# Performance work log

Measured on AMD Instinct MI355X. Metric: run time of the kernel, lower is better.

Reference implementation:

```python
import jax, jax.numpy as jnp
import numpy as np

# Standard 2D morphsnakes structuring elements (4 line filters), matching the
# repo-level global `filters` used by LSNet2.
_SE = np.zeros((4, 3, 3), dtype=np.float32)
_SE[0, 1, :] = 1.0           # horizontal line
_SE[1, :, 1] = 1.0           # vertical line
_SE[2] = np.eye(3, dtype=np.float32)          # main diagonal
_SE[3] = np.eye(3, dtype=np.float32)[::-1]    # anti-diagonal


def _dilate_stack(x, filts):
    # per-pixel: max over 3x3 window of (zero-padded x + filt), for every filter
    H, W = x.shape
    p = jnp.pad(x, 1)
    m = jnp.full((filts.shape[0], H, W), -jnp.inf, x.dtype)
    for k in range(3):
        for l in range(3):
            m = jnp.maximum(m, p[k:k + H, l:l + W][None] + filts[:, k, l][:, None, None])
    return m  # [F, H, W]


def _erode_stack(x, filts):
    # per-pixel: min over 3x3 window of (zero-padded x - filt) == -max(-(x - filt))
    H, W = x.shape
    p = jnp.pad(x, 1)
    m = jnp.full((filts.shape[0], H, W), jnp.inf, x.dtype)
    for k in range(3):
        for l in range(3):
            m = jnp.minimum(m, p[k:k + H, l:l + W][None] - filts[:, k, l][:, None, None])
    return m  # [F, H, W]


def _dilate_min(x, filts):
    return jnp.min(_dilate_stack(x, filts), axis=0)


def _erode_max(x, filts):
    return jnp.max(_erode_stack(x, filts), axis=0)


def setup_inputs() -> dict:
    key = jax.random.key(0)
    k1, k2 = jax.random.split(key)
    H = W = 2048
    inp = jax.random.uniform(k1, (H, W), dtype=jnp.float32)
    origin = jax.random.uniform(k2, (H, W), dtype=jnp.float32)
    filters = jnp.asarray(_SE)
    return {"input": inp, "origin": origin, "filters": filters}


def reference(input, origin, filters):
    x = input
    # SI o IS smoothing: dilate/min, erode/max, erode/max, dilate/min, dilate/min, erode/max
    x = _dilate_min(x, filters)
    x = _erode_max(x, filters)
    x = _erode_max(x, filters)
    x = _dilate_min(x, filters)
    x = _dilate_min(x, filters)
    x = _erode_max(x, filters)

    # balloon force with v = 1 and a flat ones(3,3) structuring element
    ones_f = jnp.ones((1, 3, 3), x.dtype)
    aux = _dilate_stack(x, ones_f)[0]
    threshold = jnp.percentile(x, 40.0)
    x = jnp.where(origin > threshold, aux, x)

    # Chan-Vese region means and update
    c0 = jnp.sum(origin * (1.0 - x)) / (jnp.sum(1.0 - x) + 1e-8)
    c1 = jnp.sum(origin * x) / (jnp.sum(x) + 1e-8)
    cv = (origin - c1) ** 2 - (origin - c0) ** 2
    x = jnp.where(cv < 0, 1.0, jnp.where(cv > 0, 0.0, x))
    return x
```

## Files before the change

### kernel.cpp

```cpp
#include <hip/hip_runtime.h>

#define HH 2048
#define WW 2048
#define NN (HH*WW)

static constexpr unsigned RANK0 = 1677721u;
static constexpr unsigned KEYLO = 0xB000u;
static constexpr unsigned KEYHI_ = 0xC000u;
static constexpr int NBINS = 4096;
static constexpr int NPART = 512;

#define TH 32
#define TW 128
#define LR 44
#define LCP 148

struct Scal {
  double c0, c1;
};

static constexpr size_t OFF_CTL    = (size_t)NN * 4;
static constexpr size_t OFF_COARSE = OFF_CTL;
static constexpr size_t OFF_UNDER  = OFF_COARSE + (size_t)NBINS * 4;
static constexpr size_t OFF_OVER   = OFF_UNDER + 4;
static constexpr size_t OFF_MIDA   = OFF_OVER + 4;
static constexpr size_t OFF_MIDB   = OFF_MIDA + 1024;
static constexpr size_t OFF_H2A    = OFF_MIDB + 1024;
static constexpr size_t OFF_H2B    = OFF_H2A + 65536ull * 4;
static constexpr size_t CTL_END    = OFF_H2B + 65536ull * 4;
static constexpr size_t CTL_BYTES  = CTL_END - OFF_CTL;
static constexpr size_t OFF_SCAL   = CTL_END;
static constexpr size_t OFF_PART   = OFF_SCAL + 64;

__device__ __forceinline__ float mx3(float a, float b, float c){ return fmaxf(fmaxf(a,b),c); }
__device__ __forceinline__ float mn3(float a, float b, float c){ return fminf(fminf(a,b),c); }

__device__ __forceinline__ unsigned keyf(float x){
  unsigned b = __float_as_uint(x);
  return (b & 0x80000000u) ? ~b : (b | 0x80000000u);
}
__device__ __forceinline__ float keyinv(unsigned k){
  unsigned b = (k & 0x80000000u) ? (k ^ 0x80000000u) : ~k;
  return __uint_as_float(b);
}

__device__ __forceinline__ unsigned excl_scan256(unsigned v, volatile unsigned* tmp, int t){
  int lane = t & 63, wv = t >> 6;
  unsigned inc = v;
  #pragma unroll
  for (int off = 1; off < 64; off <<= 1){
    unsigned u = __shfl_up(inc, off);
    if (lane >= off) inc += u;
  }
  if (lane == 63) tmp[wv] = inc;
  __syncthreads();
  unsigned wo = 0;
  #pragma unroll
  for (int w = 0; w < 4; w++) wo += (w < wv) ? tmp[w] : 0u;
  __syncthreads();
  return wo + inc - v;
}

__device__ __forceinline__ void coarse_rank(const unsigned* __restrict__ gh,
                                            const unsigned* __restrict__ under,
                                            unsigned* cres, volatile unsigned* stmp, int t){
  unsigned bins[16], loc = 0;
  #pragma unroll
  for (int i = 0; i < 16; i++){ bins[i] = gh[t*16 + i]; loc += bins[i]; }
  unsigned run = excl_scan256(loc, stmp, t) + under[0];
  #pragma unroll
  for (int i = 0; i < 16; i++){
    unsigned cc = bins[i];
    if (cc){
      if (RANK0 >= run && RANK0 - run < cc){ cres[0] = KEYLO + (unsigned)(t*16+i); cres[1] = RANK0 - run; }
      if (RANK0+1 >= run && RANK0+1 - run < cc){ cres[2] = KEYLO + (unsigned)(t*16+i); cres[3] = RANK0+1 - run; }
    }
    run += cc;
  }
  __syncthreads();
}

__device__ __forceinline__ void rank256(const unsigned* __restrict__ h, unsigned r,
                                        unsigned* res2, volatile unsigned* stmp, int t){
  unsigned c = h[t];
  unsigned ex = excl_scan256(c, stmp, t);
  if (c && r >= ex && r - ex < c){ res2[0] = (unsigned)t; res2[1] = r - ex; }
  __syncthreads();
}

__device__ __forceinline__ void loadwin3q(const float* __restrict__ src, int rowbase,
                                          int gL, int gC, int gR, float w[6]){
  float4 vp = *reinterpret_cast<const float4*>(&src[rowbase + 4*gL]);
  float4 v  = *reinterpret_cast<const float4*>(&src[rowbase + 4*gC]);
  float4 vn = *reinterpret_cast<const float4*>(&src[rowbase + 4*gR]);
  w[0] = vp.w;
  w[1]=v.x; w[2]=v.y; w[3]=v.z; w[4]=v.w;
  w[5] = vn.x;
}

__device__ __forceinline__ void morph4(bool DIL,
    const float pr[6], const float cr[6], const float nr[6], float w[4]){
  #pragma unroll
  for (int i = 0; i < 4; i++){
    if (DIL){
      float Ah = mx3(cr[i],   cr[i+1], cr[i+2]);
      float Av = mx3(pr[i+1], cr[i+1], nr[i+1]);
      float Ad = mx3(pr[i],   cr[i+1], nr[i+2]);
      float Aa = mx3(pr[i+2], cr[i+1], nr[i]);
      float tm = mx3(pr[i], pr[i+1], pr[i+2]);
      float bm = mx3(nr[i], nr[i+1], nr[i+2]);
      float M9 = mx3(tm, Ah, bm);
      w[i] = fmaxf(M9, 1.0f + fminf(fminf(Ah,Av), fminf(Ad,Aa)));
    } else {
      float Bh = mn3(cr[i],   cr[i+1], cr[i+2]);
      float Bv = mn3(pr[i+1], cr[i+1], nr[i+1]);
      float Bd = mn3(pr[i],   cr[i+1], nr[i+2]);
      float Ba = mn3(pr[i+2], cr[i+1], nr[i]);
      float tm = mn3(pr[i], pr[i+1], pr[i+2]);
      float bm = mn3(nr[i], nr[i+1], nr[i+2]);
      float m9 = mn3(tm, Bh, bm);
      w[i] = fminf(m9, fmaxf(fmaxf(Bh,Bv), fmaxf(Bd,Ba)) - 1.0f);
    }
  }
}

__global__ __launch_bounds__(256)
void fused_morph_k(const float* __restrict__ in, float* __restrict__ out,
                   unsigned* __restrict__ gh, unsigned* __restrict__ under,
                   unsigned* __restrict__ over){
  __shared__ float lds[2][LR*LCP];
  const int tilec = blockIdx.x & 15;
  const int tiler = blockIdx.x >> 4;
  const int r0 = tiler*TH, c0 = tilec*TW;

  for (int idx = threadIdx.x; idx < LR*36; idx += 256){
    int lr = idx / 36, g = idx % 36;
    int gr = r0 - 6 + lr, gc = c0 - 8 + 4*g;
    float4 v = make_float4(0.f,0.f,0.f,0.f);
    if ((unsigned)gr < (unsigned)HH && (unsigned)gc < (unsigned)WW)
      v = *reinterpret_cast<const float4*>(in + (size_t)gr*WW + gc);
    *reinterpret_cast<float4*>(&lds[0][lr*LCP + 4*g]) = v;
  }
  __syncthreads();

  const int t = threadIdx.x;
  const int g = t % 36, s = t / 36;
  const bool active = (t < 252);
  const int gL = g ? g - 1 : 0;
  const int gR = (g == 35) ? 35 : g + 1;
  const int gcBase = c0 - 8 + 4*g;
  const bool dilf[6] = {true,false,false,true,true,false};

  #pragma unroll 1
  for (int st = 0; st < 6; st++){
    const float* src = lds[st & 1];
    float*       dst = lds[(st & 1) ^ 1];
    if (active){
      const bool DIL = dilf[st];
      float r8[8][6];
      #pragma unroll
      for (int k = 0; k < 8; k++)
        loadwin3q(src, (6*s + k)*LCP, gL, g, gR, r8[k]);
      #pragma unroll
      for (int k = 0; k < 6; k++){
        float w[4];
        morph4(DIL, r8[k], r8[k+1], r8[k+2], w);
        int gr = r0 - 6 + 6*s + 1 + k;
        if ((unsigned)gr >= (unsigned)HH){
          w[0]=w[1]=w[2]=w[3]=0.f;
        } else {
          #pragma unroll
          for (int i = 0; i < 4; i++)
            if ((unsigned)(gcBase + i) >= (unsigned)WW) w[i] = 0.f;
        }
        *reinterpret_cast<float4*>(&dst[(6*s + 1 + k)*LCP + 4*g]) =
            make_float4(w[0],w[1],w[2],w[3]);
      }
    }
    __syncthreads();
  }
  unsigned* lh = reinterpret_cast<unsigned*>(&lds[1][0]);
  for (int i = threadIdx.x; i < NBINS; i += 256) lh[i] = 0;
  __syncthreads();

  unsigned uc = 0, oc = 0;
  for (int idx = threadIdx.x; idx < TH*(TW/4); idx += 256){
    int row = idx >> 5, gg = idx & 31;
    float4 v = *reinterpret_cast<const float4*>(&lds[0][(row+6)*LCP + 8 + 4*gg]);
    *reinterpret_cast<float4*>(out + (size_t)(r0+row)*WW + c0 + 4*gg) = v;
    float vv[4] = {v.x, v.y, v.z, v.w};
    #pragma unroll
    for (int i = 0; i < 4; i++){
      unsigned key = keyf(vv[i]);
      unsigned hi = key >> 16;
      if (hi >= KEYLO && hi < KEYHI_) atomicAdd(&lh[hi - KEYLO], 1u);
      else if (hi < KEYLO)            uc++;
      else                            oc++;
    }
  }
  __syncthreads();
  for (int i = threadIdx.x; i < NBINS; i += 256){
    unsigned c = lh[i];
    if (c) atomicAdd(&gh[i], c);
  }
  if (uc) atomicAdd(under, uc);
  if (oc) atomicAdd(over, oc);
}

__global__ __launch_bounds__(256)
void fine2d_k(const float* __restrict__ x,
              const unsigned* __restrict__ coarse, const unsigned* __restrict__ under,
              unsigned* __restrict__ midA, unsigned* __restrict__ midB,
              unsigned* __restrict__ h2A, unsigned* __restrict__ h2B){
  __shared__ unsigned hA[256], hB[256];
  __shared__ unsigned stmp[4], cres[4];
  const int t = threadIdx.x;
  coarse_rank(coarse, under, cres, stmp, t);
  unsigned ha = cres[0], hb = cres[2];
  bool dup = (ha == hb);
  hA[t] = 0; hB[t] = 0;
  __syncthreads();
  const int nItems = NN/4;
  for (int it = blockIdx.x*blockDim.x + t; it < nItems; it += gridDim.x*blockDim.x){
    float4 v = reinterpret_cast<const float4*>(x)[it];
    float vv[4] = {v.x, v.y, v.z, v.w};
    #pragma unroll
    for (int j = 0; j < 4; j++){
      unsigned key = keyf(vv[j]);
      unsigned hi = key >> 16;
      if (hi == ha){ atomicAdd(&hA[(key>>8)&255], 1u); atomicAdd(&h2A[key & 0xFFFFu], 1u); }
      else if (hi == hb){ atomicAdd(&hB[(key>>8)&255], 1u); atomicAdd(&h2B[key & 0xFFFFu], 1u); }
    }
  }
  __syncthreads();
  if (hA[t]) atomicAdd(&midA[t], hA[t]);
  if (!dup && hB[t]) atomicAdd(&midB[t], hB[t]);
}

__device__ __forceinline__ void load6(const float* __restrict__ p, int row, int q, float r[6]){
  if (row < 0 || row >= HH){
    r[0]=r[1]=r[2]=r[3]=r[4]=r[5]=0.f;
    return;
  }
  const float* rp = p + (size_t)row * WW;
  float4 cc = *reinterpret_cast<const float4*>(rp + q);
  r[0] = (q > 0) ? rp[q-1] : 0.f;
  r[1]=cc.x; r[2]=cc.y; r[3]=cc.z; r[4]=cc.w;
  r[5] = (q+4 < WW) ? rp[q+4] : 0.f;
}

__global__ __launch_bounds__(256)
void balloon_k(const float* __restrict__ x, const float* __restrict__ orig,
               float* __restrict__ xb,
               const unsigned* __restrict__ coarse, const unsigned* __restrict__ under,
               const unsigned* __restrict__ midA, const unsigned* __restrict__ midB,
               const unsigned* __restrict__ h2A, const unsigned* __restrict__ h2B,
               double* __restrict__ part){
  __shared__ unsigned stmp[4], cres[4], mresA[2], mresB[2], lresA[2], lresB[2];
  __shared__ double red[4][3];
  const int t = threadIdx.x;

  coarse_rank(coarse, under, cres, stmp, t);
  unsigned ha = cres[0], rA = cres[1], hb = cres[2], rB = cres[3];
  bool dupHi = (ha == hb);
  rank256(midA, rA, mresA, stmp, t);
  rank256(dupHi ? midA : midB, rB, mresB, stmp, t);
  unsigned mA = mresA[0], rA2 = mresA[1], mB = mresB[0], rB2 = mresB[1];
  rank256(h2A + (size_t)mA*256, rA2, lresA, stmp, t);
  rank256((dupHi ? h2A : h2B) + (size_t)mB*256, rB2, lresB, stmp, t);
  unsigned ka = (ha << 16) | (mA << 8) | lresA[0];
  unsigned kb = (hb << 16) | (mB << 8) | lresB[0];
  double va = (double)keyinv(ka), vb = (double)keyinv(kb);
  const double FRAC = 0.4*(double)(NN-1) - (double)RANK0;
  double thr = va + (vb - va) * FRAC;

  double s0 = 0.0, s1 = 0.0, s2 = 0.0;
  const int nItems = NN/4;
  for (int it = blockIdx.x*blockDim.x + t; it < nItems; it += gridDim.x*blockDim.x){
    int i = it >> 9;
    int q = (it & 511) << 2;
    float a[6], b[6], c[6];
    load6(x, i-1, q, a);
    load6(x, i,   q, b);
    load6(x, i+1, q, c);
    float4 og = *reinterpret_cast<const float4*>(orig + (size_t)i*WW + q);
    float ov[4] = {og.x, og.y, og.z, og.w};
    float r[4];
    #pragma unroll
    for (int j = 0; j < 4; j++){
      float M9 = mx3(mx3(a[j],a[j+1],a[j+2]), mx3(b[j],b[j+1],b[j+2]), mx3(c[j],c[j+1],c[j+2]));
      float aux = 1.0f + M9;
      float nx = ((double)ov[j] > thr) ? aux : b[j+1];
      r[j] = nx;
      s0 += (double)ov[j];
      s1 += (double)nx;
      s2 += (double)ov[j] * (double)nx;
    }
    *reinterpret_cast<float4*>(xb + (size_t)i*WW + q) = make_float4(r[0],r[1],r[2],r[3]);
  }
  for (int off = 32; off > 0; off >>= 1){
    s0 += __shfl_down(s0, off);
    s1 += __shfl_down(s1, off);
    s2 += __shfl_down(s2, off);
  }
  int lane = t & 63, wv = t >> 6;
  if (lane == 0){ red[wv][0] = s0; red[wv][1] = s1; red[wv][2] = s2; }
  __syncthreads();
  if (t == 0){
    part[blockIdx.x*3+0] = red[0][0]+red[1][0]+red[2][0]+red[3][0];
    part[blockIdx.x*3+1] = red[0][1]+red[1][1]+red[2][1]+red[3][1];
    part[blockIdx.x*3+2] = red[0][2]+red[1][2]+red[2][2]+red[3][2];
  }
}

__global__ void c0c1_k(const double* __restrict__ part, Scal* __restrict__ sc){
  int t = threadIdx.x;
  double s0 = 0, s1 = 0, s2 = 0;
  for (int b = t; b < NPART; b += 256){
    s0 += part[b*3+0]; s1 += part[b*3+1]; s2 += part[b*3+2];
  }
  for (int off = 32; off > 0; off >>= 1){
    s0 += __shfl_down(s0, off);
    s1 += __shfl_down(s1, off);
    s2 += __shfl_down(s2, off);
  }
  __shared__ double red[4][3];
  int lane = t & 63, wv = t >> 6;
  if (lane == 0){ red[wv][0] = s0; red[wv][1] = s1; red[wv][2] = s2; }
  __syncthreads();
  if (t == 0){
    double So = red[0][0]+red[1][0]+red[2][0]+red[3][0];
    double Sx = red[0][1]+red[1][1]+red[2][1]+red[3][1];
    double Sox= red[0][2]+red[1][2]+red[2][2]+red[3][2];
    sc->c0 = (So - Sox) / ((double)NN - Sx + 1e-8);
    sc->c1 = Sox / (Sx + 1e-8);
  }
}

__global__ __launch_bounds__(256)
void final_k(const float* __restrict__ orig, const float* __restrict__ xb,
             const Scal* __restrict__ sc, float* __restrict__ out){
  double c0 = sc->c0, c1 = sc->c1;
  const int nItems = NN/4;
  for (int it = blockIdx.x*blockDim.x + threadIdx.x; it < nItems; it += gridDim.x*blockDim.x){
    float4 og = reinterpret_cast<const float4*>(orig)[it];
    float4 xv = reinterpret_cast<const float4*>(xb)[it];
    float ov[4] = {og.x, og.y, og.z, og.w};
    float xx[4] = {xv.x, xv.y, xv.z, xv.w};
    float r[4];
    #pragma unroll
    for (int t = 0; t < 4; t++){
      double o = (double)ov[t];
      double d1 = o - c1, d0 = o - c0;
      double cv = d1*d1 - d0*d0;
      r[t] = (cv < 0.0) ? 1.0f : ((cv > 0.0) ? 0.0f : xx[t]);
    }
    reinterpret_cast<float4*>(out)[it] = make_float4(r[0],r[1],r[2],r[3]);
  }
}

extern "C" void kernel_launch(void* const* d_in, const int* in_sizes, int n_in,
                              void* d_out, int out_size, void* d_ws, size_t ws_size,
                              hipStream_t stream) {
  const float* input  = (const float*)d_in[0];
  const float* origin = (const float*)d_in[1];
  float* out = (float*)d_out;

  char* ws = (char*)d_ws;
  float*    bufA   = (float*)ws;
  unsigned* coarse = (unsigned*)(ws + OFF_COARSE);
  unsigned* under  = (unsigned*)(ws + OFF_UNDER);
  unsigned* over   = (unsigned*)(ws + OFF_OVER);
  unsigned* midA   = (unsigned*)(ws + OFF_MIDA);
  unsigned* midB   = (unsigned*)(ws + OFF_MIDB);
  unsigned* h2A    = (unsigned*)(ws + OFF_H2A);
  unsigned* h2B    = (unsigned*)(ws + OFF_H2B);
  Scal*     scal   = (Scal*)(ws + OFF_SCAL);
  double*   part   = (double*)(ws + OFF_PART);

  hipMemsetAsync(ws + OFF_CTL, 0, CTL_BYTES, stream);

  fused_morph_k<<<(HH/TH)*(WW/TW), 256, 0, stream>>>(input, out, coarse, under, over);
  fine2d_k<<<1024, 256, 0, stream>>>(out, coarse, under, midA, midB, h2A, h2B);
  balloon_k<<<NPART, 256, 0, stream>>>(out, origin, bufA, coarse, under,
                                       midA, midB, h2A, h2B, part);
  c0c1_k<<<1, 256, 0, stream>>>(part, scal);
  final_k<<<2048, 256, 0, stream>>>(origin, bufA, scal, out);
}
```

Before: 112.7 us.

## Fuse morphology stages in register pairs to halve LDS round-trips and barriers

Each of the three loop iterations now computes two consecutive morphology stages. The first stage is evaluated on a 10x8 register window with a 1-pixel halo, and the second stage consumes those intermediates directly from registers, so the intermediate plane is never written to and reread from shared memory. This removes three LDS passes and three block barriers. In exchange it recomputes halo cells redundantly and raises register pressure considerably (an 8x6 intermediate array plus a 10x8 input window), which may lower occupancy. The ping-pong buffer indices for the final output and the histogram are swapped to match the odd number of passes.

```diff
diff --git a/kernel.cpp b/kernel.cpp
--- a/kernel.cpp
+++ b/kernel.cpp
@@ -88,39 +88,21 @@
   __syncthreads();
 }
 
-__device__ __forceinline__ void loadwin3q(const float* __restrict__ src, int rowbase,
-                                          int gL, int gC, int gR, float w[6]){
-  float4 vp = *reinterpret_cast<const float4*>(&src[rowbase + 4*gL]);
-  float4 v  = *reinterpret_cast<const float4*>(&src[rowbase + 4*gC]);
-  float4 vn = *reinterpret_cast<const float4*>(&src[rowbase + 4*gR]);
-  w[0] = vp.w;
-  w[1]=v.x; w[2]=v.y; w[3]=v.z; w[4]=v.w;
-  w[5] = vn.x;
-}
-
-__device__ __forceinline__ void morph4(bool DIL,
-    const float pr[6], const float cr[6], const float nr[6], float w[4]){
-  #pragma unroll
-  for (int i = 0; i < 4; i++){
-    if (DIL){
-      float Ah = mx3(cr[i],   cr[i+1], cr[i+2]);
-      float Av = mx3(pr[i+1], cr[i+1], nr[i+1]);
-      float Ad = mx3(pr[i],   cr[i+1], nr[i+2]);
-      float Aa = mx3(pr[i+2], cr[i+1], nr[i]);
-      float tm = mx3(pr[i], pr[i+1], pr[i+2]);
-      float bm = mx3(nr[i], nr[i+1], nr[i+2]);
-      float M9 = mx3(tm, Ah, bm);
-      w[i] = fmaxf(M9, 1.0f + fminf(fminf(Ah,Av), fminf(Ad,Aa)));
-    } else {
-      float Bh = mn3(cr[i],   cr[i+1], cr[i+2]);
-      float Bv = mn3(pr[i+1], cr[i+1], nr[i+1]);
-      float Bd = mn3(pr[i],   cr[i+1], nr[i+2]);
-      float Ba = mn3(pr[i+2], cr[i+1], nr[i]);
-      float tm = mn3(pr[i], pr[i+1], pr[i+2]);
-      float bm = mn3(nr[i], nr[i+1], nr[i+2]);
-      float m9 = mn3(tm, Bh, bm);
-      w[i] = fminf(m9, fmaxf(fmaxf(Bh,Bv), fmaxf(Bd,Ba)) - 1.0f);
-    }
+__device__ __forceinline__ float cellm(bool DIL, const float* pr, const float* cr, const float* nr){
+  if (DIL){
+    float Ah = mx3(cr[0], cr[1], cr[2]);
+    float Av = mx3(pr[1], cr[1], nr[1]);
+    float Ad = mx3(pr[0], cr[1], nr[2]);
+    float Aa = mx3(pr[2], cr[1], nr[0]);
+    float M9 = mx3(mx3(pr[0],pr[1],pr[2]), Ah, mx3(nr[0],nr[1],nr[2]));
+    return fmaxf(M9, 1.0f + fminf(fminf(Ah,Av), fminf(Ad,Aa)));
+  } else {
+    float Bh = mn3(cr[0], cr[1], cr[2]);
+    float Bv = mn3(pr[1], cr[1], nr[1]);
+    float Bd = mn3(pr[0], cr[1], nr[2]);
+    float Ba = mn3(pr[2], cr[1], nr[0]);
+    float m9 = mn3(mn3(pr[0],pr[1],pr[2]), Bh, mn3(nr[0],nr[1],nr[2]));
+    return fminf(m9, fmaxf(fmaxf(Bh,Bv), fmaxf(Bd,Ba)) - 1.0f);
   }
 }
 
@@ -146,26 +128,51 @@
   const int t = threadIdx.x;
   const int g = t % 36, s = t / 36;
   const bool active = (t < 252);
+  const int rbase = 1 + 6*s;
   const int gL = g ? g - 1 : 0;
   const int gR = (g == 35) ? 35 : g + 1;
   const int gcBase = c0 - 8 + 4*g;
-  const bool dilf[6] = {true,false,false,true,true,false};
+  const bool pairA[3] = {true, false, true};
+  const bool pairB[3] = {false, true, false};
 
   #pragma unroll 1
-  for (int st = 0; st < 6; st++){
-    const float* src = lds[st & 1];
-    float*       dst = lds[(st & 1) ^ 1];
+  for (int p = 0; p < 3; p++){
+    const float* src = lds[p & 1];
+    float*       dst = lds[(p & 1) ^ 1];
     if (active){
-      const bool DIL = dilf[st];
-      float r8[8][6];
+      const bool DA = pairA[p], DB = pairB[p];
+      float in8[10][8];
       #pragma unroll
-      for (int k = 0; k < 8; k++)
-        loadwin3q(src, (6*s + k)*LCP, gL, g, gR, r8[k]);
+      for (int r = 0; r < 10; r++){
+        int rr = rbase - 2 + r;
+        rr = rr < 0 ? 0 : (rr > LR-1 ? LR-1 : rr);
+        const float* rp = &src[rr*LCP];
+        float4 vm = *reinterpret_cast<const float4*>(&rp[4*gL]);
+        float4 vc = *reinterpret_cast<const float4*>(&rp[4*g]);
+        float4 vn = *reinterpret_cast<const float4*>(&rp[4*gR]);
+        in8[r][0]=vm.z; in8[r][1]=vm.w;
+        in8[r][2]=vc.x; in8[r][3]=vc.y; in8[r][4]=vc.z; in8[r][5]=vc.w;
+        in8[r][6]=vn.x; in8[r][7]=vn.y;
+      }
+      float A[8][6];
+      #pragma unroll
+      for (int r = 0; r < 8; r++){
+        int gra = r0 - 6 + rbase - 1 + r;
+        bool rowOK = (unsigned)gra < (unsigned)HH;
+        #pragma unroll
+        for (int j = 0; j < 6; j++){
+          float v = cellm(DA, &in8[r][j], &in8[r+1][j], &in8[r+2][j]);
+          int gca = c0 - 9 + 4*g + j;
+          A[r][j] = (rowOK && (unsigned)gca < (unsigned)WW) ? v : 0.f;
+        }
+      }
       #pragma unroll
       for (int k = 0; k < 6; k++){
         float w[4];
-        morph4(DIL, r8[k], r8[k+1], r8[k+2], w);
-        int gr = r0 - 6 + 6*s + 1 + k;
+        #pragma unroll
+        for (int i = 0; i < 4; i++)
+          w[i] = cellm(DB, &A[k][i], &A[k+1][i], &A[k+2][i]);
+        int gr = r0 - 6 + rbase + k;
         if ((unsigned)gr >= (unsigned)HH){
           w[0]=w[1]=w[2]=w[3]=0.f;
         } else {
@@ -173,20 +180,20 @@
           for (int i = 0; i < 4; i++)
             if ((unsigned)(gcBase + i) >= (unsigned)WW) w[i] = 0.f;
         }
-        *reinterpret_cast<float4*>(&dst[(6*s + 1 + k)*LCP + 4*g]) =
+        *reinterpret_cast<float4*>(&dst[(rbase + k)*LCP + 4*g]) =
             make_float4(w[0],w[1],w[2],w[3]);
       }
     }
     __syncthreads();
   }
-  unsigned* lh = reinterpret_cast<unsigned*>(&lds[1][0]);
+  unsigned* lh = reinterpret_cast<unsigned*>(&lds[0][0]);
   for (int i = threadIdx.x; i < NBINS; i += 256) lh[i] = 0;
   __syncthreads();
 
   unsigned uc = 0, oc = 0;
   for (int idx = threadIdx.x; idx < TH*(TW/4); idx += 256){
     int row = idx >> 5, gg = idx & 31;
-    float4 v = *reinterpret_cast<const float4*>(&lds[0][(row+6)*LCP + 8 + 4*gg]);
+    float4 v = *reinterpret_cast<const float4*>(&lds[1][(row+6)*LCP + 8 + 4*gg]);
     *reinterpret_cast<float4*>(out + (size_t)(r0+row)*WW + c0 + 4*gg) = v;
     float vv[4] = {v.x, v.y, v.z, v.w};
     #pragma unroll
```

New measurement: 117.6 us. +4.3%, slower.
